# Kernel tuning notes

Measured on AMD Instinct MI355X. Metric: run time of the kernel, lower is better.

## Reference

```python
import jax, jax.numpy as jnp
import numpy as np

EPS = 1e-8  # RMSNormMultiHead default eps (forward passes self.eps)


def rms_norm_multihead(x, weight):
    # x: (B, L, H, d); normalize over last dim in float32, then scale per (H, d)
    x32 = x.astype(jnp.float32)
    normed = x32 * jax.lax.rsqrt(jnp.mean(x32 * x32, axis=-1, keepdims=True) + EPS)
    return normed.astype(x.dtype) * weight


def setup_inputs() -> dict:
    key = jax.random.key(0)
    k0, k1, k2 = jax.random.split(key, 3)
    B, L, D, H = 2, 1024, 1024, 16
    d = D // H
    X = jax.random.normal(k0, (B, L, D), dtype=jnp.float32)
    Wq = jax.random.normal(k1, (D, D), dtype=jnp.float32) * 0.02  # q_proj weight (out, in)
    Wv = jax.random.normal(k2, (D, D), dtype=jnp.float32) * 0.02  # v_proj weight (out, in)
    q_norm_w = jnp.ones((H, d), dtype=jnp.float32)
    v_norm_w = jnp.ones((H, d), dtype=jnp.float32)
    return {"X": X, "Wq": Wq, "Wv": Wv, "q_norm_w": q_norm_w, "v_norm_w": v_norm_w}


def reference(X, Wq, Wv, q_norm_w, v_norm_w):
    B, L, D = X.shape
    H, d = q_norm_w.shape
    K = X.reshape(B, L, H, d)
    Q = rms_norm_multihead((X @ Wq.T).reshape(B, L, H, d), q_norm_w)
    V = rms_norm_multihead((X @ Wv.T).reshape(B, L, H, d), v_norm_w)
    # cumulative outer-product KV state: (B, L, H, d, e)
    W = jnp.cumsum(jnp.einsum('blhd,blhe->blhde', K, V), axis=1)
    out = jnp.einsum('blhd,blhde->blhe', Q, W).reshape(B, L, D)
    return out
```

## Files before the change

### kernel.cpp

```cpp
#include <hip/hip_runtime.h>

#define BB 2
#define LL 1024
#define DD 1024
#define HH 16
#define NC 16
#define EPSF 1e-8f

typedef __attribute__((ext_vector_type(8))) short bf16x8;
typedef __attribute__((ext_vector_type(4))) float f32x4;
typedef unsigned short u16;

static __device__ inline u16 f2bf(float f) {
    unsigned int u = __builtin_bit_cast(unsigned int, f);
    u += 0x7fff + ((u >> 16) & 1);
    return (u16)(u >> 16);
}

static __device__ inline void gload_lds16(const u16* g, u16* l) {
    __builtin_amdgcn_global_load_lds((const __attribute__((address_space(1))) void*)g,
                                     (__attribute__((address_space(3))) void*)l, 16, 0, 0);
}

__global__ __launch_bounds__(256) void cvt_k(const float* __restrict__ X,
                                             const float* __restrict__ Wq,
                                             const float* __restrict__ Wv,
                                             u16* __restrict__ Xb,
                                             u16* __restrict__ Wqb,
                                             u16* __restrict__ Wvb)
{
    int i = (blockIdx.x * 256 + threadIdx.x) * 4;
    const float* s; u16* d; int off;
    if (i < 2*1024*1024)      { s = X;  d = Xb;  off = i; }
    else if (i < 3*1024*1024) { s = Wq; d = Wqb; off = i - 2*1024*1024; }
    else                      { s = Wv; d = Wvb; off = i - 3*1024*1024; }
    float4 v = *(const float4*)(s + off);
    ushort4 o;
    o.x = f2bf(v.x); o.y = f2bf(v.y); o.z = f2bf(v.z); o.w = f2bf(v.w);
    *(ushort4*)(d + off) = o;
}

__global__ __launch_bounds__(256) void gemm_fused(const u16* __restrict__ Xb,
                                                  const u16* __restrict__ Wqb,
                                                  const u16* __restrict__ Wvb,
                                                  const float* __restrict__ qw,
                                                  const float* __restrict__ vw,
                                                  u16* __restrict__ Qb,
                                                  u16* __restrict__ Vb)
{
    const int K = DD, N = DD;
    const u16* W = blockIdx.z ? Wvb : Wqb;
    const float* nw = blockIdx.z ? vw : qw;
    u16* Y = blockIdx.z ? Vb : Qb;
    __shared__ u16 As[128 * 32];
    __shared__ u16 Bs[64 * 32];
    __shared__ float Cs[128][65];

    const int tid = threadIdx.x, w = tid >> 6, lane = tid & 63;
    const int quad = lane >> 4, l16 = lane & 15;
    const int wm = w & 1, wn = w >> 1;
    const int m0 = blockIdx.y * 128, n0 = blockIdx.x * 64;
    const int lrow = lane >> 2, lcol = (lane & 3) * 8;

    const u16* gA0 = Xb + (size_t)(m0 + w*16 + lrow) * K + lcol;
    const u16* gA1 = gA0 + (size_t)64 * K;
    const u16* gB0 = W + (size_t)(n0 + w*16 + lrow) * K + lcol;
    u16* lA0 = &As[(w*16) * 32];
    u16* lA1 = &As[(64 + w*16) * 32];
    u16* lB0 = &Bs[(w*16) * 32];

    f32x4 acc[4][2] = {};
    for (int k0 = 0; k0 < K; k0 += 32) {
        gload_lds16(gA0 + k0, lA0);
        gload_lds16(gA1 + k0, lA1);
        gload_lds16(gB0 + k0, lB0);
        __syncthreads();
        bf16x8 af[4], bf[2];
        #pragma unroll
        for (int i = 0; i < 4; ++i)
            af[i] = *(const bf16x8*)&As[(wm*64 + i*16 + l16) * 32 + quad*8];
        #pragma unroll
        for (int j = 0; j < 2; ++j)
            bf[j] = *(const bf16x8*)&Bs[(wn*32 + j*16 + l16) * 32 + quad*8];
        #pragma unroll
        for (int i = 0; i < 4; ++i)
            #pragma unroll
            for (int j = 0; j < 2; ++j)
                acc[i][j] = __builtin_amdgcn_mfma_f32_16x16x32_bf16(af[i], bf[j], acc[i][j], 0, 0, 0);
        __syncthreads();
    }

    #pragma unroll
    for (int i = 0; i < 4; ++i)
        #pragma unroll
        for (int j = 0; j < 2; ++j)
            #pragma unroll
            for (int r = 0; r < 4; ++r)
                Cs[wm*64 + i*16 + quad*4 + r][wn*32 + j*16 + l16] = acc[i][j][r];
    __syncthreads();

    const int row = tid >> 1, half = tid & 1;
    float vals[32];
    float ss = 0.f;
    #pragma unroll
    for (int c = 0; c < 32; c += 4) {
        float4 v = *(const float4*)&Cs[row][half*32 + c];
        vals[c] = v.x; vals[c+1] = v.y; vals[c+2] = v.z; vals[c+3] = v.w;
        ss += v.x*v.x + v.y*v.y + v.z*v.z + v.w*v.w;
    }
    ss += __shfl_xor(ss, 1, 64);
    const float scale = rsqrtf(ss * (1.f/64.f) + EPSF);
    const float* wp = nw + n0 + half*32;
    u16* yp = Y + (size_t)(m0 + row) * N + n0 + half*32;
    #pragma unroll
    for (int c = 0; c < 32; c += 4) {
        ushort4 o;
        o.x = f2bf(vals[c]   * scale * wp[c]);
        o.y = f2bf(vals[c+1] * scale * wp[c+1]);
        o.z = f2bf(vals[c+2] * scale * wp[c+2]);
        o.w = f2bf(vals[c+3] * scale * wp[c+3]);
        *(ushort4*)(yp + c) = o;
    }
}

__global__ __launch_bounds__(256) void chunk_kv(const u16* __restrict__ Xb,
                                                const u16* __restrict__ Vb,
                                                float* __restrict__ S)
{
    const int c = blockIdx.x & 15, bh = blockIdx.x >> 4;
    const int h = bh & 15, b = bh >> 4;
    __shared__ u16 Kt[64][72];
    __shared__ u16 Vt[64][72];
    const int tid = threadIdx.x;
    {
        const int row = tid >> 2, q = tid & 3;
        size_t gbase = (size_t)(b*LL + c*64 + row) * DD + h*64 + q*16;
        u16 kk[16], vv[16];
        #pragma unroll
        for (int i = 0; i < 16; i += 4) {
            *(ushort4*)&kk[i] = *(const ushort4*)(Xb + gbase + i);
            *(ushort4*)&vv[i] = *(const ushort4*)(Vb + gbase + i);
        }
        #pragma unroll
        for (int i = 0; i < 16; ++i) {
            Kt[q*16 + i][row] = kk[i];
            Vt[q*16 + i][row] = vv[i];
        }
    }
    __syncthreads();
    const int w = tid >> 6, lane = tid & 63, quad = lane >> 4, l16 = lane & 15;
    const int me = (w & 1) * 32, nd = (w >> 1) * 32;
    f32x4 acc[2][2] = {};
    #pragma unroll
    for (int k0 = 0; k0 < 64; k0 += 32) {
        bf16x8 av[2], bv[2];
        #pragma unroll
        for (int i = 0; i < 2; ++i)
            av[i] = *(const bf16x8*)&Vt[me + i*16 + l16][k0 + quad*8];
        #pragma unroll
        for (int j = 0; j < 2; ++j)
            bv[j] = *(const bf16x8*)&Kt[nd + j*16 + l16][k0 + quad*8];
        #pragma unroll
        for (int i = 0; i < 2; ++i)
            #pragma unroll
            for (int j = 0; j < 2; ++j)
                acc[i][j] = __builtin_amdgcn_mfma_f32_16x16x32_bf16(av[i], bv[j], acc[i][j], 0, 0, 0);
    }
    float* Sp = S + (size_t)blockIdx.x * 4096;
    #pragma unroll
    for (int i = 0; i < 2; ++i)
        #pragma unroll
        for (int j = 0; j < 2; ++j)
            #pragma unroll
            for (int r = 0; r < 4; ++r)
                Sp[(me + i*16 + quad*4 + r) * 64 + nd + j*16 + l16] = acc[i][j][r];
}

__global__ __launch_bounds__(256) void cumsum_k(float* __restrict__ S)
{
    int bh = blockIdx.x >> 4;
    int p  = (blockIdx.x & 15) * 256 + threadIdx.x;
    float* base = S + (size_t)bh * NC * 4096 + p;
    float run = 0.f;
    #pragma unroll
    for (int c = 0; c < NC; ++c) {
        float v = base[c * 4096];
        base[c * 4096] = run;
        run += v;
    }
}

__global__ __launch_bounds__(256) void out_k(const u16* __restrict__ Xb,
                                             const u16* __restrict__ Qb,
                                             const u16* __restrict__ Vb,
                                             const float* __restrict__ S,
                                             float* __restrict__ out)
{
    const int c = blockIdx.x & 15, bh = blockIdx.x >> 4;
    const int h = bh & 15, b = bh >> 4;
    __shared__ u16 Qs[64][72];
    __shared__ u16 Ks[64][72];
    __shared__ u16 Vt[64][72];
    __shared__ u16 St[64][72];
    __shared__ u16 Ps[64][72];
    const int tid = threadIdx.x;
    {
        const int row = tid >> 2, q = tid & 3;
        size_t gbase = (size_t)(b*LL + c*64 + row) * DD + h*64 + q*16;
        u16 qv[16], kv[16], vv[16];
        #pragma unroll
        for (int i = 0; i < 16; i += 4) {
            *(ushort4*)&qv[i] = *(const ushort4*)(Qb + gbase + i);
            *(ushort4*)&kv[i] = *(const ushort4*)(Xb + gbase + i);
            *(ushort4*)&vv[i] = *(const ushort4*)(Vb + gbase + i);
        }
        #pragma unroll
        for (int i = 0; i < 16; ++i) {
            Qs[row][q*16 + i] = qv[i];
            Ks[row][q*16 + i] = kv[i];
            Vt[q*16 + i][row] = vv[i];
        }
        const float* sp = S + (size_t)blockIdx.x * 4096 + row*64 + q*16;
        #pragma unroll
        for (int i = 0; i < 16; i += 4) {
            float4 sv = *(const float4*)(sp + i);
            St[row][q*16 + i]     = f2bf(sv.x);
            St[row][q*16 + i + 1] = f2bf(sv.y);
            St[row][q*16 + i + 2] = f2bf(sv.z);
            St[row][q*16 + i + 3] = f2bf(sv.w);
        }
    }
    __syncthreads();
    const int w = tid >> 6, lane = tid & 63, quad = lane >> 4, l16 = lane & 15;
    const int mo = (w & 1) * 32, no = (w >> 1) * 32;

    {
        f32x4 pacc[2][2] = {};
        #pragma unroll
        for (int k0 = 0; k0 < 64; k0 += 32) {
            bf16x8 aq[2], bk[2];
            #pragma unroll
            for (int i = 0; i < 2; ++i)
                aq[i] = *(const bf16x8*)&Qs[mo + i*16 + l16][k0 + quad*8];
            #pragma unroll
            for (int j = 0; j < 2; ++j)
                bk[j] = *(const bf16x8*)&Ks[no + j*16 + l16][k0 + quad*8];
            #pragma unroll
            for (int i = 0; i < 2; ++i)
                #pragma unroll
                for (int j = 0; j < 2; ++j)
                    pacc[i][j] = __builtin_amdgcn_mfma_f32_16x16x32_bf16(aq[i], bk[j], pacc[i][j], 0, 0, 0);
        }
        #pragma unroll
        for (int i = 0; i < 2; ++i)
            #pragma unroll
            for (int j = 0; j < 2; ++j)
                #pragma unroll
                for (int r = 0; r < 4; ++r) {
                    int l  = mo + i*16 + quad*4 + r;
                    int lp = no + j*16 + l16;
                    Ps[l][lp] = (lp <= l) ? f2bf(pacc[i][j][r]) : (u16)0;
                }
    }
    __syncthreads();

    f32x4 acc[2][2] = {};
    #pragma unroll
    for (int k0 = 0; k0 < 64; k0 += 32) {
        bf16x8 a1[2], b1[2], a2[2], b2[2];
        #pragma unroll
        for (int i = 0; i < 2; ++i) {
            a1[i] = *(const bf16x8*)&Ps[mo + i*16 + l16][k0 + quad*8];
            a2[i] = *(const bf16x8*)&Qs[mo + i*16 + l16][k0 + quad*8];
        }
        #pragma unroll
        for (int j = 0; j < 2; ++j) {
            b1[j] = *(const bf16x8*)&Vt[no + j*16 + l16][k0 + quad*8];
            b2[j] = *(const bf16x8*)&St[no + j*16 + l16][k0 + quad*8];
        }
        #pragma unroll
        for (int i = 0; i < 2; ++i)
            #pragma unroll
            for (int j = 0; j < 2; ++j) {
                acc[i][j] = __builtin_amdgcn_mfma_f32_16x16x32_bf16(a1[i], b1[j], acc[i][j], 0, 0, 0);
                acc[i][j] = __builtin_amdgcn_mfma_f32_16x16x32_bf16(a2[i], b2[j], acc[i][j], 0, 0, 0);
            }
    }
    float* op = out + (size_t)(b*LL + c*64) * DD + h*64;
    #pragma unroll
    for (int i = 0; i < 2; ++i)
        #pragma unroll
        for (int j = 0; j < 2; ++j)
            #pragma unroll
            for (int r = 0; r < 4; ++r)
                op[(size_t)(mo + i*16 + quad*4 + r) * DD + no + j*16 + l16] = acc[i][j][r];
}

extern "C" void kernel_launch(void* const* d_in, const int* in_sizes, int n_in,
                              void* d_out, int out_size, void* d_ws, size_t ws_size,
                              hipStream_t stream) {
    const float* X  = (const float*)d_in[0];
    const float* Wq = (const float*)d_in[1];
    const float* Wv = (const float*)d_in[2];
    const float* qw = (const float*)d_in[3];
    const float* vw = (const float*)d_in[4];
    float* out = (float*)d_out;

    u16* Xb  = (u16*)d_ws;
    u16* Wqb = Xb  + (size_t)2*1024*1024;
    u16* Wvb = Wqb + (size_t)1024*1024;
    u16* Qb  = Wvb + (size_t)1024*1024;
    u16* Vb  = Qb  + (size_t)2*1024*1024;
    float* S = (float*)(Vb + (size_t)2*1024*1024);

    cvt_k<<<4096, 256, 0, stream>>>(X, Wq, Wv, Xb, Wqb, Wvb);
    gemm_fused<<<dim3(16, 16, 2), 256, 0, stream>>>(Xb, Wqb, Wvb, qw, vw, Qb, Vb);
    chunk_kv<<<BB*HH*NC, 256, 0, stream>>>(Xb, Vb, S);
    cumsum_k<<<BB*HH*NC, 256, 0, stream>>>(S);
    out_k<<<BB*HH*NC, 256, 0, stream>>>(Xb, Qb, Vb, S, out);
}
```

Baseline: 108.7 us.

## Fuse chunk KV state and prefix scan into one kernel, register-level RMSNorm epilogue

Replaces the separate chunk_kv and cumsum_k kernels with a single kv_scan kernel. Each block walks all 16 chunks for one (b,h) 32x32 sub-tile, keeps the running state in MFMA accumulators and writes the exclusive prefix state as bf16. This removes one launch and the fp32 state round trip, but cuts the grid to 128 blocks that run serial chunk loops. The GEMM epilogue now does RMSNorm directly from accumulators using lane shuffles, with each wave covering the full 64-column head, which drops the fp32 LDS staging tile. out_k reuses the Ks buffer for the masked score matrix, which saves LDS.

After: 110.4 us. Within noise of the previous version (+1.6%).

```diff
diff --git a/kernel.cpp b/kernel.cpp
--- a/kernel.cpp
+++ b/kernel.cpp
@@ -54,11 +54,9 @@
     u16* Y = blockIdx.z ? Vb : Qb;
     __shared__ u16 As[128 * 32];
     __shared__ u16 Bs[64 * 32];
-    __shared__ float Cs[128][65];
 
     const int tid = threadIdx.x, w = tid >> 6, lane = tid & 63;
     const int quad = lane >> 4, l16 = lane & 15;
-    const int wm = w & 1, wn = w >> 1;
     const int m0 = blockIdx.y * 128, n0 = blockIdx.x * 64;
     const int lrow = lane >> 2, lcol = (lane & 3) * 8;
 
@@ -69,131 +67,112 @@
     u16* lA1 = &As[(64 + w*16) * 32];
     u16* lB0 = &Bs[(w*16) * 32];
 
-    f32x4 acc[4][2] = {};
+    f32x4 acc[2][4] = {};
     for (int k0 = 0; k0 < K; k0 += 32) {
         gload_lds16(gA0 + k0, lA0);
         gload_lds16(gA1 + k0, lA1);
         gload_lds16(gB0 + k0, lB0);
         __syncthreads();
-        bf16x8 af[4], bf[2];
-        #pragma unroll
-        for (int i = 0; i < 4; ++i)
-            af[i] = *(const bf16x8*)&As[(wm*64 + i*16 + l16) * 32 + quad*8];
-        #pragma unroll
-        for (int j = 0; j < 2; ++j)
-            bf[j] = *(const bf16x8*)&Bs[(wn*32 + j*16 + l16) * 32 + quad*8];
-        #pragma unroll
-        for (int i = 0; i < 4; ++i)
-            #pragma unroll
-            for (int j = 0; j < 2; ++j)
-                acc[i][j] = __builtin_amdgcn_mfma_f32_16x16x32_bf16(af[i], bf[j], acc[i][j], 0, 0, 0);
-        __syncthreads();
-    }
-
-    #pragma unroll
-    for (int i = 0; i < 4; ++i)
-        #pragma unroll
-        for (int j = 0; j < 2; ++j)
-            #pragma unroll
-            for (int r = 0; r < 4; ++r)
-                Cs[wm*64 + i*16 + quad*4 + r][wn*32 + j*16 + l16] = acc[i][j][r];
-    __syncthreads();
-
-    const int row = tid >> 1, half = tid & 1;
-    float vals[32];
-    float ss = 0.f;
-    #pragma unroll
-    for (int c = 0; c < 32; c += 4) {
-        float4 v = *(const float4*)&Cs[row][half*32 + c];
-        vals[c] = v.x; vals[c+1] = v.y; vals[c+2] = v.z; vals[c+3] = v.w;
-        ss += v.x*v.x + v.y*v.y + v.z*v.z + v.w*v.w;
-    }
-    ss += __shfl_xor(ss, 1, 64);
-    const float scale = rsqrtf(ss * (1.f/64.f) + EPSF);
-    const float* wp = nw + n0 + half*32;
-    u16* yp = Y + (size_t)(m0 + row) * N + n0 + half*32;
-    #pragma unroll
-    for (int c = 0; c < 32; c += 4) {
-        ushort4 o;
-        o.x = f2bf(vals[c]   * scale * wp[c]);
-        o.y = f2bf(vals[c+1] * scale * wp[c+1]);
-        o.z = f2bf(vals[c+2] * scale * wp[c+2]);
-        o.w = f2bf(vals[c+3] * scale * wp[c+3]);
-        *(ushort4*)(yp + c) = o;
-    }
-}
-
-__global__ __launch_bounds__(256) void chunk_kv(const u16* __restrict__ Xb,
-                                                const u16* __restrict__ Vb,
-                                                float* __restrict__ S)
-{
-    const int c = blockIdx.x & 15, bh = blockIdx.x >> 4;
+        bf16x8 af[2], bfr[4];
+        #pragma unroll
+        for (int i = 0; i < 2; ++i)
+            af[i] = *(const bf16x8*)&As[(w*32 + i*16 + l16) * 32 + quad*8];
+        #pragma unroll
+        for (int j = 0; j < 4; ++j)
+            bfr[j] = *(const bf16x8*)&Bs[(j*16 + l16) * 32 + quad*8];
+        #pragma unroll
+        for (int i = 0; i < 2; ++i)
+            #pragma unroll
+            for (int j = 0; j < 4; ++j)
+                acc[i][j] = __builtin_amdgcn_mfma_f32_16x16x32_bf16(af[i], bfr[j], acc[i][j], 0, 0, 0);
+        __syncthreads();
+    }
+
+    float wv[4];
+    #pragma unroll
+    for (int j = 0; j < 4; ++j) wv[j] = nw[n0 + j*16 + l16];
+    #pragma unroll
+    for (int i = 0; i < 2; ++i) {
+        float ss[4];
+        #pragma unroll
+        for (int r = 0; r < 4; ++r) {
+            float s = 0.f;
+            #pragma unroll
+            for (int j = 0; j < 4; ++j) s += acc[i][j][r] * acc[i][j][r];
+            ss[r] = s;
+        }
+        #pragma unroll
+        for (int off = 1; off < 16; off <<= 1)
+            #pragma unroll
+            for (int r = 0; r < 4; ++r) ss[r] += __shfl_xor(ss[r], off, 64);
+        float sc[4];
+        #pragma unroll
+        for (int r = 0; r < 4; ++r) sc[r] = rsqrtf(ss[r] * (1.f/64.f) + EPSF);
+        #pragma unroll
+        for (int r = 0; r < 4; ++r) {
+            u16* yp = Y + (size_t)(m0 + w*32 + i*16 + quad*4 + r) * N + n0;
+            #pragma unroll
+            for (int j = 0; j < 4; ++j)
+                yp[j*16 + l16] = f2bf(acc[i][j][r] * sc[r] * wv[j]);
+        }
+    }
+}
+
+__global__ __launch_bounds__(256) void kv_scan(const u16* __restrict__ Xb,
+                                               const u16* __restrict__ Vb,
+                                               u16* __restrict__ S)
+{
+    const int t = blockIdx.x & 3, bh = blockIdx.x >> 2;
+    const int et = t & 1, dt = t >> 1;
     const int h = bh & 15, b = bh >> 4;
-    __shared__ u16 Kt[64][72];
-    __shared__ u16 Vt[64][72];
-    const int tid = threadIdx.x;
-    {
-        const int row = tid >> 2, q = tid & 3;
-        size_t gbase = (size_t)(b*LL + c*64 + row) * DD + h*64 + q*16;
-        u16 kk[16], vv[16];
-        #pragma unroll
-        for (int i = 0; i < 16; i += 4) {
-            *(ushort4*)&kk[i] = *(const ushort4*)(Xb + gbase + i);
-            *(ushort4*)&vv[i] = *(const ushort4*)(Vb + gbase + i);
-        }
-        #pragma unroll
-        for (int i = 0; i < 16; ++i) {
-            Kt[q*16 + i][row] = kk[i];
-            Vt[q*16 + i][row] = vv[i];
-        }
-    }
-    __syncthreads();
-    const int w = tid >> 6, lane = tid & 63, quad = lane >> 4, l16 = lane & 15;
-    const int me = (w & 1) * 32, nd = (w >> 1) * 32;
-    f32x4 acc[2][2] = {};
-    #pragma unroll
-    for (int k0 = 0; k0 < 64; k0 += 32) {
-        bf16x8 av[2], bv[2];
-        #pragma unroll
-        for (int i = 0; i < 2; ++i)
-            av[i] = *(const bf16x8*)&Vt[me + i*16 + l16][k0 + quad*8];
-        #pragma unroll
-        for (int j = 0; j < 2; ++j)
-            bv[j] = *(const bf16x8*)&Kt[nd + j*16 + l16][k0 + quad*8];
-        #pragma unroll
-        for (int i = 0; i < 2; ++i)
-            #pragma unroll
-            for (int j = 0; j < 2; ++j)
-                acc[i][j] = __builtin_amdgcn_mfma_f32_16x16x32_bf16(av[i], bv[j], acc[i][j], 0, 0, 0);
-    }
-    float* Sp = S + (size_t)blockIdx.x * 4096;
-    #pragma unroll
-    for (int i = 0; i < 2; ++i)
-        #pragma unroll
-        for (int j = 0; j < 2; ++j)
-            #pragma unroll
-            for (int r = 0; r < 4; ++r)
-                Sp[(me + i*16 + quad*4 + r) * 64 + nd + j*16 + l16] = acc[i][j][r];
-}
-
-__global__ __launch_bounds__(256) void cumsum_k(float* __restrict__ S)
-{
-    int bh = blockIdx.x >> 4;
-    int p  = (blockIdx.x & 15) * 256 + threadIdx.x;
-    float* base = S + (size_t)bh * NC * 4096 + p;
-    float run = 0.f;
-    #pragma unroll
+    __shared__ u16 Kt[32][72];
+    __shared__ u16 Vt[32][72];
+    const int tid = threadIdx.x, w = tid >> 6, lane = tid & 63;
+    const int quad = lane >> 4, l16 = lane & 15;
+    const int esub = (w & 1) * 16, dsub = (w >> 1) * 16;
+    const int row = tid >> 2, q = tid & 3;
+
+    const u16* gK = Xb + (size_t)(b*LL + row) * DD + h*64 + dt*32 + q*8;
+    const u16* gV = Vb + (size_t)(b*LL + row) * DD + h*64 + et*32 + q*8;
+
+    ushort4 kr[2], vr[2];
+    kr[0] = *(const ushort4*)(gK);     kr[1] = *(const ushort4*)(gK + 4);
+    vr[0] = *(const ushort4*)(gV);     vr[1] = *(const ushort4*)(gV + 4);
+
+    f32x4 acc = {};
     for (int c = 0; c < NC; ++c) {
-        float v = base[c * 4096];
-        base[c * 4096] = run;
-        run += v;
+        #pragma unroll
+        for (int i = 0; i < 4; ++i) {
+            Kt[q*8 + i][row]     = ((const u16*)&kr[0])[i];
+            Kt[q*8 + 4 + i][row] = ((const u16*)&kr[1])[i];
+            Vt[q*8 + i][row]     = ((const u16*)&vr[0])[i];
+            Vt[q*8 + 4 + i][row] = ((const u16*)&vr[1])[i];
+        }
+        __syncthreads();
+        if (c + 1 < NC) {
+            const u16* nK = gK + (size_t)(c+1)*64*DD;
+            const u16* nV = gV + (size_t)(c+1)*64*DD;
+            kr[0] = *(const ushort4*)(nK); kr[1] = *(const ushort4*)(nK + 4);
+            vr[0] = *(const ushort4*)(nV); vr[1] = *(const ushort4*)(nV + 4);
+        }
+        u16* Sp = S + ((size_t)bh * NC + c) * 4096;
+        #pragma unroll
+        for (int r = 0; r < 4; ++r)
+            Sp[(et*32 + esub + quad*4 + r) * 64 + dt*32 + dsub + l16] = f2bf(acc[r]);
+        #pragma unroll
+        for (int k0 = 0; k0 < 64; k0 += 32) {
+            bf16x8 av = *(const bf16x8*)&Vt[esub + l16][k0 + quad*8];
+            bf16x8 bv = *(const bf16x8*)&Kt[dsub + l16][k0 + quad*8];
+            acc = __builtin_amdgcn_mfma_f32_16x16x32_bf16(av, bv, acc, 0, 0, 0);
+        }
+        __syncthreads();
     }
 }
 
 __global__ __launch_bounds__(256) void out_k(const u16* __restrict__ Xb,
                                              const u16* __restrict__ Qb,
                                              const u16* __restrict__ Vb,
-                                             const float* __restrict__ S,
+                                             const u16* __restrict__ S,
                                              float* __restrict__ out)
 {
     const int c = blockIdx.x & 15, bh = blockIdx.x >> 4;
@@ -202,66 +181,56 @@
     __shared__ u16 Ks[64][72];
     __shared__ u16 Vt[64][72];
     __shared__ u16 St[64][72];
-    __shared__ u16 Ps[64][72];
     const int tid = threadIdx.x;
     {
         const int row = tid >> 2, q = tid & 3;
         size_t gbase = (size_t)(b*LL + c*64 + row) * DD + h*64 + q*16;
-        u16 qv[16], kv[16], vv[16];
+        u16 vv[16];
         #pragma unroll
         for (int i = 0; i < 16; i += 4) {
-            *(ushort4*)&qv[i] = *(const ushort4*)(Qb + gbase + i);
-            *(ushort4*)&kv[i] = *(const ushort4*)(Xb + gbase + i);
+            *(ushort4*)&Qs[row][q*16 + i] = *(const ushort4*)(Qb + gbase + i);
+            *(ushort4*)&Ks[row][q*16 + i] = *(const ushort4*)(Xb + gbase + i);
             *(ushort4*)&vv[i] = *(const ushort4*)(Vb + gbase + i);
         }
         #pragma unroll
-        for (int i = 0; i < 16; ++i) {
-            Qs[row][q*16 + i] = qv[i];
-            Ks[row][q*16 + i] = kv[i];
+        for (int i = 0; i < 16; ++i)
             Vt[q*16 + i][row] = vv[i];
-        }
-        const float* sp = S + (size_t)blockIdx.x * 4096 + row*64 + q*16;
-        #pragma unroll
-        for (int i = 0; i < 16; i += 4) {
-            float4 sv = *(const float4*)(sp + i);
-            St[row][q*16 + i]     = f2bf(sv.x);
-            St[row][q*16 + i + 1] = f2bf(sv.y);
-            St[row][q*16 + i + 2] = f2bf(sv.z);
-            St[row][q*16 + i + 3] = f2bf(sv.w);
-        }
+        const u16* sp = S + ((size_t)bh * NC + c) * 4096 + row*64 + q*16;
+        #pragma unroll
+        for (int i = 0; i < 16; i += 4)
+            *(ushort4*)&St[row][q*16 + i] = *(const ushort4*)(sp + i);
     }
     __syncthreads();
     const int w = tid >> 6, lane = tid & 63, quad = lane >> 4, l16 = lane & 15;
     const int mo = (w & 1) * 32, no = (w >> 1) * 32;
 
-    {
-        f32x4 pacc[2][2] = {};
-        #pragma unroll
-        for (int k0 = 0; k0 < 64; k0 += 32) {
-            bf16x8 aq[2], bk[2];
-            #pragma unroll
-            for (int i = 0; i < 2; ++i)
-                aq[i] = *(const bf16x8*)&Qs[mo + i*16 + l16][k0 + quad*8];
+    f32x4 pacc[2][2] = {};
+    #pragma unroll
+    for (int k0 = 0; k0 < 64; k0 += 32) {
+        bf16x8 aq[2], bk[2];
+        #pragma unroll
+        for (int i = 0; i < 2; ++i)
+            aq[i] = *(const bf16x8*)&Qs[mo + i*16 + l16][k0 + quad*8];
+        #pragma unroll
+        for (int j = 0; j < 2; ++j)
+            bk[j] = *(const bf16x8*)&Ks[no + j*16 + l16][k0 + quad*8];
+        #pragma unroll
+        for (int i = 0; i < 2; ++i)
             #pragma unroll
             for (int j = 0; j < 2; ++j)
-                bk[j] = *(const bf16x8*)&Ks[no + j*16 + l16][k0 + quad*8];
-            #pragma unroll
-            for (int i = 0; i < 2; ++i)
-                #pragma unroll
-                for (int j = 0; j < 2; ++j)
-                    pacc[i][j] = __builtin_amdgcn_mfma_f32_16x16x32_bf16(aq[i], bk[j], pacc[i][j], 0, 0, 0);
-        }
-        #pragma unroll
-        for (int i = 0; i < 2; ++i)
-            #pragma unroll
-            for (int j = 0; j < 2; ++j)
-                #pragma unroll
-                for (int r = 0; r < 4; ++r) {
-                    int l  = mo + i*16 + quad*4 + r;
-                    int lp = no + j*16 + l16;
-                    Ps[l][lp] = (lp <= l) ? f2bf(pacc[i][j][r]) : (u16)0;
-                }
-    }
+                pacc[i][j] = __builtin_amdgcn_mfma_f32_16x16x32_bf16(aq[i], bk[j], pacc[i][j], 0, 0, 0);
+    }
+    __syncthreads();
+    #pragma unroll
+    for (int i = 0; i < 2; ++i)
+        #pragma unroll
+        for (int j = 0; j < 2; ++j)
+            #pragma unroll
+            for (int r = 0; r < 4; ++r) {
+                int l  = mo + i*16 + quad*4 + r;
+                int lp = no + j*16 + l16;
+                Ks[l][lp] = (lp <= l) ? f2bf(pacc[i][j][r]) : (u16)0;
+            }
     __syncthreads();
 
     f32x4 acc[2][2] = {};
@@ -270,7 +239,7 @@
         bf16x8 a1[2], b1[2], a2[2], b2[2];
         #pragma unroll
         for (int i = 0; i < 2; ++i) {
-            a1[i] = *(const bf16x8*)&Ps[mo + i*16 + l16][k0 + quad*8];
+            a1[i] = *(const bf16x8*)&Ks[mo + i*16 + l16][k0 + quad*8];
             a2[i] = *(const bf16x8*)&Qs[mo + i*16 + l16][k0 + quad*8];
         }
         #pragma unroll
@@ -311,11 +280,10 @@
     u16* Wvb = Wqb + (size_t)1024*1024;
     u16* Qb  = Wvb + (size_t)1024*1024;
     u16* Vb  = Qb  + (size_t)2*1024*1024;
-    float* S = (float*)(Vb + (size_t)2*1024*1024);
+    u16* S   = Vb  + (size_t)2*1024*1024;
 
     cvt_k<<<4096, 256, 0, stream>>>(X, Wq, Wv, Xb, Wqb, Wvb);
     gemm_fused<<<dim3(16, 16, 2), 256, 0, stream>>>(Xb, Wqb, Wvb, qw, vw, Qb, Vb);
-    chunk_kv<<<BB*HH*NC, 256, 0, stream>>>(Xb, Vb, S);
-    cumsum_k<<<BB*HH*NC, 256, 0, stream>>>(S);
+    kv_scan<<<128, 256, 0, stream>>>(Xb, Vb, S);
     out_k<<<BB*HH*NC, 256, 0, stream>>>(Xb, Qb, Vb, S, out);
 }
```
